# Optimization experiments

Measured on AMD Instinct MI355X. Metric: run time of the kernel, lower is better.

The kernel has to match this reference:

```python
import math
import jax, jax.numpy as jnp
import numpy as np

ALPH = 0.8

def setup_inputs() -> dict:
    key = jax.random.key(0)
    k1, k2 = jax.random.split(key)
    B, C, N, T = 64, 64, 500, 48
    x = jax.random.normal(k1, (B, C, N, T), dtype=jnp.float32)
    s = jax.random.uniform(k2, (N, N), dtype=jnp.float32)
    return {"x": x, "s": s}

def reference(x, s):
    # x: [B, C, N, T], s: [N, N]
    B, C, N, T = x.shape
    # Row sums of the (never materialized) [N*T, N*T] supra-laplacian:
    # block row i, node v -> s.sum(axis=1)[v] + (T-1-i)*alph
    s_rowsum = s.sum(axis=1)                              # [N]
    time_term = (T - 1 - jnp.arange(T, dtype=jnp.float32)) * ALPH  # [T]
    rowsum = (time_term[:, None] + s_rowsum[None, :]).reshape(-1)  # [T*N], k = i*N+v
    # Faithful to original: x flattened as [B, C, N*T] (k = n*T + t), multiplied
    # elementwise by rowsum[k] (the 'bcn,nm->bcn' einsum reduces to this).
    x_window = x.reshape(B, C, N * T)
    x_window = jax.nn.relu(x_window * rowsum / math.sqrt(C))
    adj_dyn = jax.nn.softmax(x_window, axis=-1)            # [B, C, N*T]
    x_w_s = adj_dyn.reshape(B, C, N, T).sum(-1)            # [B, C, N]
    gram = jnp.einsum('bcn,bcm->bnm', x_w_s, x_w_s)        # [B, N, N]
    A_l = jax.nn.softmax(jax.nn.relu(gram) / math.sqrt(C), axis=-1)
    return A_l
```

## Files before the change

### kernel.cpp

```cpp
#include <hip/hip_runtime.h>
#include <math.h>

#define NN 500
#define TT 48
#define NT 24000
#define NF4 6000

__global__ void k_srow(const float* __restrict__ s, float* __restrict__ srow) {
    int r = blockIdx.x;
    int l = threadIdx.x;
    float v = 0.f;
    for (int j = l; j < NN; j += 64) v += s[r * NN + j];
    #pragma unroll
    for (int o = 32; o; o >>= 1) v += __shfl_xor(v, o);
    if (l == 0) srow[r] = v;
}

__global__ void k_rs(const float* __restrict__ srow, float* __restrict__ rs) {
    int k = blockIdx.x * 256 + threadIdx.x;
    if (k < NT) {
        int i = k / NN;
        int v = k - i * NN;
        rs[k] = (float)(TT - 1 - i) * 0.8f + srow[v];
    }
}

__launch_bounds__(512, 4)
__global__ void k_p1(const float* __restrict__ x, const float* __restrict__ rs,
                     float* __restrict__ xws) {
    __shared__ float p[6144];
    __shared__ float redm[8], reds[8];
    int bc = blockIdx.x;
    int tid = threadIdx.x;
    int w = tid >> 6, l = tid & 63;
    int f0 = w * 768 + l;

    const float4* xp = (const float4*)x + (size_t)bc * NF4;
    const float4* rp = (const float4*)rs;

    float y[48];
    float m = 0.f;
    #pragma unroll
    for (int i = 0; i < 12; i++) {
        int f = f0 + i * 64;
        float4 xv = make_float4(0.f, 0.f, 0.f, 0.f);
        float4 rv = xv;
        if (f < NF4) { xv = xp[f]; rv = rp[f]; }
        float4 yv;
        yv.x = fmaxf(xv.x * rv.x * 0.125f, 0.f);
        yv.y = fmaxf(xv.y * rv.y * 0.125f, 0.f);
        yv.z = fmaxf(xv.z * rv.z * 0.125f, 0.f);
        yv.w = fmaxf(xv.w * rv.w * 0.125f, 0.f);
        y[4 * i + 0] = yv.x; y[4 * i + 1] = yv.y;
        y[4 * i + 2] = yv.z; y[4 * i + 3] = yv.w;
        m = fmaxf(m, fmaxf(fmaxf(yv.x, yv.y), fmaxf(yv.z, yv.w)));
    }

    #pragma unroll
    for (int o = 32; o; o >>= 1) m = fmaxf(m, __shfl_xor(m, o));
    if (l == 0) redm[w] = m;
    __syncthreads();
    float M = redm[0];
    #pragma unroll
    for (int i = 1; i < 8; i++) M = fmaxf(M, redm[i]);

    float tot = 0.f;
    #pragma unroll
    for (int i = 0; i < 12; i++) {
        int f = f0 + i * 64;
        float sf = 0.f;
        if (f < NF4) {
            sf = __expf(y[4 * i + 0] - M) + __expf(y[4 * i + 1] - M)
               + __expf(y[4 * i + 2] - M) + __expf(y[4 * i + 3] - M);
        }
        p[f0 + i * 64] = sf;
        tot += sf;
    }
    #pragma unroll
    for (int o = 32; o; o >>= 1) tot += __shfl_xor(tot, o);
    if (l == 0) reds[w] = tot;
    __syncthreads();
    float Z = 0.f;
    #pragma unroll
    for (int i = 0; i < 8; i++) Z += reds[i];

    if (tid < NN) {
        const float* pp = p + tid * 12;
        float sn = 0.f;
        #pragma unroll
        for (int j = 0; j < 12; j++) sn += pp[j];
        xws[(size_t)bc * NN + tid] = sn / Z;
    }
}

__launch_bounds__(512, 2)
__global__ void k_p2(const float* __restrict__ xws, float* __restrict__ out) {
    __shared__ __align__(16) float Xs[64 * NN + 64];
    int b = blockIdx.y;
    int rt8 = blockIdx.x;
    int tid = threadIdx.x;

    const float4* src4 = (const float4*)(xws + (size_t)b * 64 * NN);
    #pragma unroll
    for (int i = 0; i < 16; i++) {
        int idx = tid + i * 512;
        if (idx < 8000) ((float4*)Xs)[idx] = src4[idx];
    }
    if (tid < 64) Xs[64 * NN + tid] = 0.f;
    __syncthreads();

    int rt = tid >> 6, cx = tid & 63;
    int r0 = rt8 * 64 + rt * 8;
    int cb0 = cx * 4, cb1 = cx * 4 + 256;

    float acc[8][8];
    #pragma unroll
    for (int i = 0; i < 8; i++)
        #pragma unroll
        for (int j = 0; j < 8; j++) acc[i][j] = 0.f;

    #pragma unroll 4
    for (int c = 0; c < 64; c++) {
        const float* row = Xs + c * NN;
        float4 a0 = *(const float4*)(row + r0);
        float4 a1 = *(const float4*)(row + r0 + 4);
        float4 b0 = *(const float4*)(row + cb0);
        float4 b1 = *(const float4*)(row + cb1);
        float av[8] = {a0.x, a0.y, a0.z, a0.w, a1.x, a1.y, a1.z, a1.w};
        float bv[8] = {b0.x, b0.y, b0.z, b0.w, b1.x, b1.y, b1.z, b1.w};
        #pragma unroll
        for (int i = 0; i < 8; i++)
            #pragma unroll
            for (int j = 0; j < 8; j++)
                acc[i][j] = fmaf(av[i], bv[j], acc[i][j]);
    }

    bool c1v = (cx <= 60);
    size_t ob = (size_t)b * (NN * NN);
    #pragma unroll 1
    for (int ri = 0; ri < 8; ri++) {
        int r = r0 + ri;
        if (r >= NN) break;
        float u[8];
        #pragma unroll
        for (int j = 0; j < 8; j++) u[j] = fmaxf(acc[ri][j], 0.f) * 0.125f;
        float mx = fmaxf(fmaxf(u[0], u[1]), fmaxf(u[2], u[3]));
        if (c1v) mx = fmaxf(mx, fmaxf(fmaxf(u[4], u[5]), fmaxf(u[6], u[7])));
        #pragma unroll
        for (int o = 32; o; o >>= 1) mx = fmaxf(mx, __shfl_xor(mx, o));

        float e[8];
        float es = 0.f;
        #pragma unroll
        for (int j = 0; j < 4; j++) { e[j] = __expf(u[j] - mx); es += e[j]; }
        if (c1v) {
            #pragma unroll
            for (int j = 4; j < 8; j++) { e[j] = __expf(u[j] - mx); es += e[j]; }
        }
        #pragma unroll
        for (int o = 32; o; o >>= 1) es += __shfl_xor(es, o);
        float inv = 1.f / es;

        float4 w0 = make_float4(e[0] * inv, e[1] * inv, e[2] * inv, e[3] * inv);
        *(float4*)(out + ob + (size_t)r * NN + cb0) = w0;
        if (c1v) {
            float4 w1 = make_float4(e[4] * inv, e[5] * inv, e[6] * inv, e[7] * inv);
            *(float4*)(out + ob + (size_t)r * NN + cb1) = w1;
        }
    }
}

extern "C" void kernel_launch(void* const* d_in, const int* in_sizes, int n_in,
                              void* d_out, int out_size, void* d_ws, size_t ws_size,
                              hipStream_t stream) {
    const float* x = (const float*)d_in[0];
    const float* s = (const float*)d_in[1];
    float* out = (float*)d_out;
    float* wsf = (float*)d_ws;

    float* srow = wsf;
    float* rs   = wsf + 1024;
    float* xws  = wsf + 32768;

    k_srow<<<NN, 64, 0, stream>>>(s, srow);
    k_rs<<<(NT + 255) / 256, 256, 0, stream>>>(srow, rs);
    k_p1<<<64 * 64, 512, 0, stream>>>(x, rs, xws);
    dim3 g2(8, 64);
    k_p2<<<g2, 512, 0, stream>>>(xws, out);
}
```

Baseline: 169.3 us.

## Use online per-float4 softmax in p1 and chunk LDS staging in p2

In the row-softmax kernel, each thread now computes a local max and exp-sum per float4 right after loading, and keeps 24 scalars in place of 48 values. The later pass only rescales those partial sums by exp(local max minus global max). The out-of-range loads are clamped and masked, which removes the branch. The gram kernel now stages X into shared memory in two 32-channel chunks, which halves LDS use and raises launch bounds to 4 blocks per CU, at the cost of an extra sync and reload phase.

```diff
diff --git a/kernel.cpp b/kernel.cpp
--- a/kernel.cpp
+++ b/kernel.cpp
@@ -38,22 +38,25 @@
     const float4* xp = (const float4*)x + (size_t)bc * NF4;
     const float4* rp = (const float4*)rs;
 
-    float y[48];
+    float sf[12], ml[12];
     float m = 0.f;
     #pragma unroll
     for (int i = 0; i < 12; i++) {
         int f = f0 + i * 64;
-        float4 xv = make_float4(0.f, 0.f, 0.f, 0.f);
-        float4 rv = xv;
-        if (f < NF4) { xv = xp[f]; rv = rp[f]; }
-        float4 yv;
-        yv.x = fmaxf(xv.x * rv.x * 0.125f, 0.f);
-        yv.y = fmaxf(xv.y * rv.y * 0.125f, 0.f);
-        yv.z = fmaxf(xv.z * rv.z * 0.125f, 0.f);
-        yv.w = fmaxf(xv.w * rv.w * 0.125f, 0.f);
-        y[4 * i + 0] = yv.x; y[4 * i + 1] = yv.y;
-        y[4 * i + 2] = yv.z; y[4 * i + 3] = yv.w;
-        m = fmaxf(m, fmaxf(fmaxf(yv.x, yv.y), fmaxf(yv.z, yv.w)));
+        int fc = (f < NF4) ? f : (NF4 - 1);
+        float msk = (f < NF4) ? 1.f : 0.f;
+        float4 xv = xp[fc];
+        float4 rv = rp[fc];
+        float y0 = fmaxf(xv.x * rv.x * 0.125f, 0.f);
+        float y1 = fmaxf(xv.y * rv.y * 0.125f, 0.f);
+        float y2 = fmaxf(xv.z * rv.z * 0.125f, 0.f);
+        float y3 = fmaxf(xv.w * rv.w * 0.125f, 0.f);
+        float mm = fmaxf(fmaxf(y0, y1), fmaxf(y2, y3));
+        float sfi = __expf(y0 - mm) + __expf(y1 - mm)
+                  + __expf(y2 - mm) + __expf(y3 - mm);
+        ml[i] = mm * msk;
+        sf[i] = sfi * msk;
+        m = fmaxf(m, ml[i]);
     }
 
     #pragma unroll
@@ -67,14 +70,9 @@
     float tot = 0.f;
     #pragma unroll
     for (int i = 0; i < 12; i++) {
-        int f = f0 + i * 64;
-        float sf = 0.f;
-        if (f < NF4) {
-            sf = __expf(y[4 * i + 0] - M) + __expf(y[4 * i + 1] - M)
-               + __expf(y[4 * i + 2] - M) + __expf(y[4 * i + 3] - M);
-        }
-        p[f0 + i * 64] = sf;
-        tot += sf;
+        float cf = sf[i] * __expf(ml[i] - M);
+        p[f0 + i * 64] = cf;
+        tot += cf;
     }
     #pragma unroll
     for (int o = 32; o; o >>= 1) tot += __shfl_xor(tot, o);
@@ -93,21 +91,12 @@
     }
 }
 
-__launch_bounds__(512, 2)
+__launch_bounds__(512, 4)
 __global__ void k_p2(const float* __restrict__ xws, float* __restrict__ out) {
-    __shared__ __align__(16) float Xs[64 * NN + 64];
+    __shared__ __align__(16) float Xs[32 * NN + 16];
     int b = blockIdx.y;
     int rt8 = blockIdx.x;
     int tid = threadIdx.x;
-
-    const float4* src4 = (const float4*)(xws + (size_t)b * 64 * NN);
-    #pragma unroll
-    for (int i = 0; i < 16; i++) {
-        int idx = tid + i * 512;
-        if (idx < 8000) ((float4*)Xs)[idx] = src4[idx];
-    }
-    if (tid < 64) Xs[64 * NN + tid] = 0.f;
-    __syncthreads();
 
     int rt = tid >> 6, cx = tid & 63;
     int r0 = rt8 * 64 + rt * 8;
@@ -119,20 +108,32 @@
         #pragma unroll
         for (int j = 0; j < 8; j++) acc[i][j] = 0.f;
 
-    #pragma unroll 4
-    for (int c = 0; c < 64; c++) {
-        const float* row = Xs + c * NN;
-        float4 a0 = *(const float4*)(row + r0);
-        float4 a1 = *(const float4*)(row + r0 + 4);
-        float4 b0 = *(const float4*)(row + cb0);
-        float4 b1 = *(const float4*)(row + cb1);
-        float av[8] = {a0.x, a0.y, a0.z, a0.w, a1.x, a1.y, a1.z, a1.w};
-        float bv[8] = {b0.x, b0.y, b0.z, b0.w, b1.x, b1.y, b1.z, b1.w};
+    for (int cbk = 0; cbk < 2; cbk++) {
+        const float4* src4 = (const float4*)(xws + ((size_t)b * 64 + 32 * cbk) * NN);
+        __syncthreads();
         #pragma unroll
-        for (int i = 0; i < 8; i++)
+        for (int i = 0; i < 8; i++) {
+            int idx = tid + i * 512;
+            if (idx < 4000) ((float4*)Xs)[idx] = src4[idx];
+        }
+        if (tid < 16) Xs[32 * NN + tid] = 0.f;
+        __syncthreads();
+
+        #pragma unroll 4
+        for (int c = 0; c < 32; c++) {
+            const float* row = Xs + c * NN;
+            float4 a0 = *(const float4*)(row + r0);
+            float4 a1 = *(const float4*)(row + r0 + 4);
+            float4 b0 = *(const float4*)(row + cb0);
+            float4 b1 = *(const float4*)(row + cb1);
+            float av[8] = {a0.x, a0.y, a0.z, a0.w, a1.x, a1.y, a1.z, a1.w};
+            float bv[8] = {b0.x, b0.y, b0.z, b0.w, b1.x, b1.y, b1.z, b1.w};
             #pragma unroll
-            for (int j = 0; j < 8; j++)
-                acc[i][j] = fmaf(av[i], bv[j], acc[i][j]);
+            for (int i = 0; i < 8; i++)
+                #pragma unroll
+                for (int j = 0; j < 8; j++)
+                    acc[i][j] = fmaf(av[i], bv[j], acc[i][j]);
+        }
     }
 
     bool c1v = (cx <= 60);
```

Measured after the change: 169.5 us. Within noise of the previous version (+0.1%).
